# Kernel optimization log

Measured on AMD Instinct MI355X. Metric: run time of the kernel, lower is better.

Reference implementation:

```python
import jax, jax.numpy as jnp
import numpy as np

B, N, D = 4, 4096, 1024


def setup_inputs() -> dict:
    key = jax.random.key(0)
    ks = jax.random.split(key, 7)
    s = 1.0 / np.sqrt(D)
    return {
        "x": jax.random.normal(ks[0], (B, N, D), dtype=jnp.float32),
        "Wq": jax.random.uniform(ks[1], (D, D), jnp.float32, -s, s),
        "bq": jax.random.uniform(ks[2], (D,), jnp.float32, -s, s),
        "Wk": jax.random.uniform(ks[3], (D, D), jnp.float32, -s, s),
        "bk": jax.random.uniform(ks[4], (D,), jnp.float32, -s, s),
        "Wv": jax.random.uniform(ks[5], (D, D), jnp.float32, -s, s),
        "bv": jax.random.uniform(ks[6], (D,), jnp.float32, -s, s),
    }


def reference(x, Wq, bq, Wk, bk, Wv, bv):
    # Projections (nn.Linear: x @ W.T + b; here W stored as [in, out])
    Q = x @ Wq + bq
    K = x @ Wk + bk
    V = x @ Wv + bv
    Qp = jax.nn.elu(Q) + 1.0  # positive feature map
    Kp = jax.nn.elu(K) + 1.0
    KV = jnp.einsum('bnd,bne->bde', Kp, V)          # [B, D, D]
    numerator = jnp.einsum('bnd,bde->bne', Qp, KV)  # [B, N, D]
    K_sum = Kp.sum(axis=1)                           # [B, D]
    norm = jnp.einsum('bnd,bd->bn', Qp, K_sum)[..., None]
    eps = 1e-6
    return numerator / (norm + eps)
```

## Files before the change

### kernel.cpp

```cpp
#include <hip/hip_runtime.h>
#include <hip/hip_bf16.h>
#include <cstdint>

typedef __bf16 bf16x8 __attribute__((ext_vector_type(8)));
typedef float  f32x4  __attribute__((ext_vector_type(4)));
typedef unsigned short u16x8 __attribute__((ext_vector_type(8)));

__device__ __forceinline__ unsigned short f2bf(float f) {
  __hip_bfloat16 h = __float2bfloat16(f);
  return __builtin_bit_cast(unsigned short, h);
}
__device__ __forceinline__ float bf2f(unsigned short u) {
  return __builtin_bit_cast(float, (unsigned)u << 16);
}

#define GL2LDS16(gp, lp)                                                      \
  __builtin_amdgcn_global_load_lds(                                           \
      (const __attribute__((address_space(1))) unsigned int*)(gp),            \
      (__attribute__((address_space(3))) unsigned int*)(lp), 16, 0, 0)

#define SBAR                                                                  \
  {                                                                           \
    __builtin_amdgcn_s_barrier();                                             \
    __builtin_amdgcn_sched_barrier(0);                                        \
  }
#define WAITV(n)                                                              \
  {                                                                           \
    asm volatile("s_waitcnt vmcnt(" #n ")" ::: "memory");                     \
    __builtin_amdgcn_sched_barrier(0);                                        \
  }
#define WAITL0                                                                \
  {                                                                           \
    asm volatile("s_waitcnt lgkmcnt(0)" ::: "memory");                        \
    __builtin_amdgcn_sched_barrier(0);                                        \
  }

template <int MODE>
__global__ __launch_bounds__(1024, 4) void gemm256w(
    const unsigned short* __restrict__ A, long long lda, long long aOffZ,
    const unsigned short* __restrict__ B, long long ldb, long long bOffZ,
    void* __restrict__ C, long long ldc, long long cOffZ,
    const float* __restrict__ bias, const float* __restrict__ bias2,
    int K) {
  __shared__ __attribute__((aligned(16))) char lds[3 * 32768];
  const int t = threadIdx.x;
  const int wave = t >> 6, lane = t & 63;
  const int wm = wave >> 2, wn = wave & 3;
  const int fr = lane & 15, fq = lane >> 4;

  const int gx = gridDim.x, gy = gridDim.y;
  int flat = blockIdx.y * gx + blockIdx.x;
  const int total = gx * gy;
  if ((total & 7) == 0) flat = (flat & 7) * (total >> 3) + (flat >> 3);
  int bx, by;
  if (MODE == 1) {
    bx = flat / gy;
    by = flat - bx * gy;
  } else {
    bx = flat % gx;
    by = flat / gx;
  }
  const int m0 = by * 256, n0 = bx * 256;

  const long long z = blockIdx.z;
  long long aBase, bBase;
  if (MODE == 3) {
    const long long koff = (z & 3) * 4096 + (z >> 2) * 1024;
    aBase = koff;
    bBase = koff;
  } else {
    aBase = z * aOffZ;
    bBase = z * bOffZ;
  }
  const unsigned short* Az = A + aBase;
  const unsigned short* Bz = B + bBase;

  const unsigned short* gA;
  const unsigned short* gB;
  {
    int d = t * 16;
    int l = d ^ (((d >> 7) & 3) << 4);
    int row = l >> 6, kel = (l & 63) >> 1;
    gA = Az + (long long)(m0 + row) * lda + kel;
    gB = Bz + (long long)(n0 + row) * ldb + kel;
  }

  const int slotx = (fr >> 1) & 3;
  const int acore = wm * 4096 + fr * 64 + ((fq ^ slotx) << 4);
  const int bcore = 16384 + wn * 4096 + fr * 64 + ((fq ^ slotx) << 4);

  f32x4 acc[4][4];
#pragma unroll
  for (int i = 0; i < 4; ++i)
#pragma unroll
    for (int j = 0; j < 4; ++j) acc[i][j] = (f32x4){0.f, 0.f, 0.f, 0.f};

  const int NT = K >> 5;

  auto stage = [&](int tile) {
    char* sb = lds + (tile % 3) * 32768 + wave * 1024;
    const int k0 = tile << 5;
    GL2LDS16(gA + k0, sb);
    GL2LDS16(gB + k0, sb + 16384);
  };

  stage(0);
  stage(1);
  WAITV(2);
  SBAR;

  bf16x8 av[4], bv[4];
  for (int tt = 0; tt < NT - 2; ++tt) {
    const char* sb = lds + (tt % 3) * 32768;
    stage(tt + 2);
#pragma unroll
    for (int i = 0; i < 4; ++i) {
      av[i] = *(const bf16x8*)(sb + acore + i * 1024);
      bv[i] = *(const bf16x8*)(sb + bcore + i * 1024);
    }
    WAITL0;
    __builtin_amdgcn_s_setprio(1);
#pragma unroll
    for (int mi = 0; mi < 4; ++mi)
#pragma unroll
      for (int ni = 0; ni < 4; ++ni)
        acc[mi][ni] = __builtin_amdgcn_mfma_f32_16x16x32_bf16(
            av[mi], bv[ni], acc[mi][ni], 0, 0, 0);
    __builtin_amdgcn_s_setprio(0);
    WAITV(2);
    SBAR;
  }
  {
    const char* sb = lds + ((NT - 2) % 3) * 32768;
#pragma unroll
    for (int i = 0; i < 4; ++i) {
      av[i] = *(const bf16x8*)(sb + acore + i * 1024);
      bv[i] = *(const bf16x8*)(sb + bcore + i * 1024);
    }
    WAITL0;
#pragma unroll
    for (int mi = 0; mi < 4; ++mi)
#pragma unroll
      for (int ni = 0; ni < 4; ++ni)
        acc[mi][ni] = __builtin_amdgcn_mfma_f32_16x16x32_bf16(
            av[mi], bv[ni], acc[mi][ni], 0, 0, 0);
    WAITV(0);
    SBAR;
  }
  {
    const char* sb = lds + ((NT - 1) % 3) * 32768;
#pragma unroll
    for (int i = 0; i < 4; ++i) {
      av[i] = *(const bf16x8*)(sb + acore + i * 1024);
      bv[i] = *(const bf16x8*)(sb + bcore + i * 1024);
    }
    WAITL0;
#pragma unroll
    for (int mi = 0; mi < 4; ++mi)
#pragma unroll
      for (int ni = 0; ni < 4; ++ni)
        acc[mi][ni] = __builtin_amdgcn_mfma_f32_16x16x32_bf16(
            av[mi], bv[ni], acc[mi][ni], 0, 0, 0);
  }

  unsigned short* Cu = (unsigned short*)C + z * cOffZ;
  const bool lower = (m0 < 1024);
#pragma unroll
  for (int mi = 0; mi < 4; ++mi) {
    const int rbase = m0 + wm * 64 + mi * 16 + fq * 4;
    float rb[4];
#pragma unroll
    for (int j = 0; j < 4; ++j)
      if (MODE == 1) rb[j] = lower ? bias[rbase + j] : bias2[rbase - 1024 + j];
#pragma unroll
    for (int ni = 0; ni < 4; ++ni) {
      const int c = n0 + wn * 64 + ni * 16 + fr;
      float cb = 0.f;
      if (MODE == 0) cb = bias[c];
#pragma unroll
      for (int j = 0; j < 4; ++j) {
        float v = acc[mi][ni][j];
        if (MODE == 0) v += cb;
        if (MODE == 1) v += rb[j];
        if (MODE == 0 || (MODE == 1 && lower))
          v = (v > 0.f) ? v + 1.f : __expf(v);
        Cu[(long long)(rbase + j) * ldc + c] = f2bf(v);
      }
    }
  }
}

__global__ __launch_bounds__(512, 2) void gemm_num(
    const unsigned short* __restrict__ A, long long aOffZ,
    const unsigned short* __restrict__ B, long long bOffZ,
    float* __restrict__ C, long long cOffZ,
    const float* __restrict__ norm, long long normOffZ) {
  const long long lda = 1024, ldb = 1024, ldc = 1024;
  const int K = 1024;
  __shared__ __attribute__((aligned(16))) char lds[2 * 65536];
  const int t = threadIdx.x;
  const int wave = t >> 6, lane = t & 63;
  const int wm = wave >> 2, wn = wave & 3;
  const int fr = lane & 15, fq = lane >> 4;

  const int gx = gridDim.x, gy = gridDim.y;
  int flat = blockIdx.y * gx + blockIdx.x;
  const int total = gx * gy;
  if ((total & 7) == 0) flat = (flat & 7) * (total >> 3) + (flat >> 3);
  const int bx = flat % gx, by = flat / gx;
  const int m0 = by * 256, n0 = bx * 256;

  const long long z = blockIdx.z;
  const unsigned short* Az = A + z * aOffZ;
  const unsigned short* Bz = B + z * bOffZ;

  const unsigned short* gA[2];
  const unsigned short* gB[2];
#pragma unroll
  for (int c = 0; c < 2; ++c) {
    int d = c * 8192 + t * 16;
    int l = d ^ (((d >> 7) & 3) << 4);
    int row = l >> 6, kel = (l & 63) >> 1;
    gA[c] = Az + (long long)(m0 + row) * lda + kel;
    gB[c] = Bz + (long long)(n0 + row) * ldb + kel;
  }

  const int slotx = (fr >> 1) & 3;
  const int acore = wm * 8192 + fr * 64 + ((fq ^ slotx) << 4);
  const int bcore = wn * 4096 + fr * 64 + ((fq ^ slotx) << 4);

  f32x4 acc[8][4];
#pragma unroll
  for (int i = 0; i < 8; ++i)
#pragma unroll
    for (int j = 0; j < 4; ++j) acc[i][j] = (f32x4){0.f, 0.f, 0.f, 0.f};

  const int NT = K >> 6;

  auto stage_sub = [&](int tile, int which) {
    char* dst = lds + (tile & 1) * 65536 + which * 16384 + wave * 1024;
    const int kofs = (tile << 6) + ((which >> 1) << 5);
    if (which & 1) {
      GL2LDS16(gB[0] + kofs, dst);
      GL2LDS16(gB[1] + kofs, dst + 8192);
    } else {
      GL2LDS16(gA[0] + kofs, dst);
      GL2LDS16(gA[1] + kofs, dst + 8192);
    }
  };

  stage_sub(0, 0);
  stage_sub(0, 1);
  stage_sub(0, 2);
  stage_sub(0, 3);
  WAITV(4);
  SBAR;

  bf16x8 av[4], bv0[4], bv1[4];
  for (int tt = 0; tt < NT - 1; ++tt) {
    const char* bufp = lds + (tt & 1) * 65536;
#pragma unroll
    for (int i = 0; i < 4; ++i) {
      av[i] = *(const bf16x8*)(bufp + acore + i * 1024);
      bv0[i] = *(const bf16x8*)(bufp + 16384 + bcore + i * 1024);
    }
    stage_sub(tt + 1, 0);
    SBAR;
    WAITL0;
    __builtin_amdgcn_s_setprio(1);
#pragma unroll
    for (int mi = 0; mi < 4; ++mi)
#pragma unroll
      for (int ni = 0; ni < 4; ++ni)
        acc[mi][ni] = __builtin_amdgcn_mfma_f32_16x16x32_bf16(
            av[mi], bv0[ni], acc[mi][ni], 0, 0, 0);
    __builtin_amdgcn_s_setprio(0);
    SBAR;
#pragma unroll
    for (int i = 0; i < 4; ++i)
      av[i] = *(const bf16x8*)(bufp + acore + (4 + i) * 1024);
    stage_sub(tt + 1, 1);
    SBAR;
    WAITL0;
    __builtin_amdgcn_s_setprio(1);
#pragma unroll
    for (int mi = 0; mi < 4; ++mi)
#pragma unroll
      for (int ni = 0; ni < 4; ++ni)
        acc[4 + mi][ni] = __builtin_amdgcn_mfma_f32_16x16x32_bf16(
            av[mi], bv0[ni], acc[4 + mi][ni], 0, 0, 0);
    __builtin_amdgcn_s_setprio(0);
    WAITV(4);
    SBAR;
#pragma unroll
    for (int i = 0; i < 4; ++i) {
      av[i] = *(const bf16x8*)(bufp + 32768 + acore + i * 1024);
      bv1[i] = *(const bf16x8*)(bufp + 49152 + bcore + i * 1024);
    }
    stage_sub(tt + 1, 2);
    SBAR;
    WAITL0;
    __builtin_amdgcn_s_setprio(1);
#pragma unroll
    for (int mi = 0; mi < 4; ++mi)
#pragma unroll
      for (int ni = 0; ni < 4; ++ni)
        acc[mi][ni] = __builtin_amdgcn_mfma_f32_16x16x32_bf16(
            av[mi], bv1[ni], acc[mi][ni], 0, 0, 0);
    __builtin_amdgcn_s_setprio(0);
    SBAR;
#pragma unroll
    for (int i = 0; i < 4; ++i)
      av[i] = *(const bf16x8*)(bufp + 32768 + acore + (4 + i) * 1024);
    stage_sub(tt + 1, 3);
    SBAR;
    WAITL0;
    __builtin_amdgcn_s_setprio(1);
#pragma unroll
    for (int mi = 0; mi < 4; ++mi)
#pragma unroll
      for (int ni = 0; ni < 4; ++ni)
        acc[4 + mi][ni] = __builtin_amdgcn_mfma_f32_16x16x32_bf16(
            av[mi], bv1[ni], acc[4 + mi][ni], 0, 0, 0);
    __builtin_amdgcn_s_setprio(0);
    WAITV(4);
    SBAR;
  }
  {
    const char* bufp = lds + ((NT - 1) & 1) * 65536;
#pragma unroll
    for (int i = 0; i < 4; ++i) {
      av[i] = *(const bf16x8*)(bufp + acore + i * 1024);
      bv0[i] = *(const bf16x8*)(bufp + 16384 + bcore + i * 1024);
    }
    SBAR;
    WAITL0;
#pragma unroll
    for (int mi = 0; mi < 4; ++mi)
#pragma unroll
      for (int ni = 0; ni < 4; ++ni)
        acc[mi][ni] = __builtin_amdgcn_mfma_f32_16x16x32_bf16(
            av[mi], bv0[ni], acc[mi][ni], 0, 0, 0);
    SBAR;
#pragma unroll
    for (int i = 0; i < 4; ++i)
      av[i] = *(const bf16x8*)(bufp + acore + (4 + i) * 1024);
    SBAR;
    WAITL0;
#pragma unroll
    for (int mi = 0; mi < 4; ++mi)
#pragma unroll
      for (int ni = 0; ni < 4; ++ni)
        acc[4 + mi][ni] = __builtin_amdgcn_mfma_f32_16x16x32_bf16(
            av[mi], bv0[ni], acc[4 + mi][ni], 0, 0, 0);
    WAITV(0);
    SBAR;
#pragma unroll
    for (int i = 0; i < 4; ++i) {
      av[i] = *(const bf16x8*)(bufp + 32768 + acore + i * 1024);
      bv1[i] = *(const bf16x8*)(bufp + 49152 + bcore + i * 1024);
    }
    WAITL0;
#pragma unroll
    for (int mi = 0; mi < 4; ++mi)
#pragma unroll
      for (int ni = 0; ni < 4; ++ni)
        acc[mi][ni] = __builtin_amdgcn_mfma_f32_16x16x32_bf16(
            av[mi], bv1[ni], acc[mi][ni], 0, 0, 0);
#pragma unroll
    for (int i = 0; i < 4; ++i)
      av[i] = *(const bf16x8*)(bufp + 32768 + acore + (4 + i) * 1024);
    WAITL0;
#pragma unroll
    for (int mi = 0; mi < 4; ++mi)
#pragma unroll
      for (int ni = 0; ni < 4; ++ni)
        acc[4 + mi][ni] = __builtin_amdgcn_mfma_f32_16x16x32_bf16(
            av[mi], bv1[ni], acc[4 + mi][ni], 0, 0, 0);
  }

  const float* nrmz = norm + z * normOffZ;
  float* Cf = C + z * cOffZ;
#pragma unroll
  for (int mi = 0; mi < 8; ++mi) {
    const int rbase = m0 + wm * 128 + mi * 16 + fq * 4;
    float nv[4];
#pragma unroll
    for (int j = 0; j < 4; ++j) nv[j] = nrmz[rbase + j];
#pragma unroll
    for (int ni = 0; ni < 4; ++ni) {
      const int c = n0 + wn * 64 + ni * 16 + fr;
#pragma unroll
      for (int j = 0; j < 4; ++j)
        Cf[(long long)(rbase + j) * ldc + c] = acc[mi][ni][j] / nv[j];
    }
  }
}

__global__ __launch_bounds__(256) void reduce_kvt(
    const unsigned short* __restrict__ P, unsigned short* __restrict__ KVt) {
  const long long i = ((long long)blockIdx.x * 256 + threadIdx.x) * 8;
  const int b = (int)(i >> 20);
  const long long ed = i & ((1ll << 20) - 1);
  float s[8] = {0.f, 0.f, 0.f, 0.f, 0.f, 0.f, 0.f, 0.f};
#pragma unroll
  for (int ks = 0; ks < 4; ++ks) {
    u16x8 v = *(const u16x8*)(P + ((long long)(ks * 4 + b) << 20) + ed);
#pragma unroll
    for (int j = 0; j < 8; ++j) s[j] += bf2f(v[j]);
  }
  u16x8 o;
#pragma unroll
  for (int j = 0; j < 8; ++j) o[j] = f2bf(s[j]);
  *(u16x8*)(KVt + i) = o;
}

__global__ __launch_bounds__(256) void transpose_w(
    const float* __restrict__ W, unsigned short* __restrict__ WT) {
  __shared__ float tile[32][33];
  const int tx = threadIdx.x & 31, ty = threadIdx.x >> 5;
  const int i0 = blockIdx.y * 32, o0 = blockIdx.x * 32;
#pragma unroll
  for (int s = 0; s < 32; s += 8)
    tile[ty + s][tx] = W[(long long)(i0 + ty + s) * 1024 + o0 + tx];
  __syncthreads();
#pragma unroll
  for (int s = 0; s < 32; s += 8)
    WT[(long long)(o0 + ty + s) * 1024 + i0 + tx] = f2bf(tile[tx][ty + s]);
}

__global__ __launch_bounds__(256) void convert_x(
    const float4* __restrict__ in, uint2* __restrict__ out, int n4) {
  const int stride = gridDim.x * blockDim.x;
  for (int i = blockIdx.x * blockDim.x + threadIdx.x; i < n4; i += stride) {
    float4 v = in[i];
    uint2 o;
    o.x = (unsigned)f2bf(v.x) | ((unsigned)f2bf(v.y) << 16);
    o.y = (unsigned)f2bf(v.z) | ((unsigned)f2bf(v.w) << 16);
    out[i] = o;
  }
}

__global__ __launch_bounds__(256) void ksum_kernel(
    const unsigned short* __restrict__ KpT, float* __restrict__ Ksum) {
  const int gw = (blockIdx.x * 256 + threadIdx.x) >> 6;
  const int lane = threadIdx.x & 63;
  const int d = gw >> 2, b = gw & 3;
  const unsigned short* p = KpT + (long long)d * 16384 + b * 4096 + lane * 8;
  float s = 0.f;
#pragma unroll
  for (int it = 0; it < 8; ++it) {
    u16x8 v = *(const u16x8*)(p + it * 512);
#pragma unroll
    for (int j = 0; j < 8; ++j) s += bf2f(v[j]);
  }
#pragma unroll
  for (int o = 32; o > 0; o >>= 1) s += __shfl_down(s, o, 64);
  if (lane == 0) Ksum[b * 1024 + d] = s;
}

__global__ __launch_bounds__(256) void norm_kernel(
    const unsigned short* __restrict__ Qp, const float* __restrict__ Ksum,
    float* __restrict__ nrm) {
  const int gw = (blockIdx.x * 256 + threadIdx.x) >> 6;
  const int lane = threadIdx.x & 63;
  const int b = gw >> 12;
  const unsigned short* q = Qp + (long long)gw * 1024 + lane * 8;
  const float* ks = Ksum + b * 1024 + lane * 8;
  float s = 0.f;
#pragma unroll
  for (int it = 0; it < 2; ++it) {
    u16x8 v = *(const u16x8*)(q + it * 512);
    float4 k0 = *(const float4*)(ks + it * 512);
    float4 k1 = *(const float4*)(ks + it * 512 + 4);
    s += bf2f(v[0]) * k0.x + bf2f(v[1]) * k0.y + bf2f(v[2]) * k0.z +
         bf2f(v[3]) * k0.w + bf2f(v[4]) * k1.x + bf2f(v[5]) * k1.y +
         bf2f(v[6]) * k1.z + bf2f(v[7]) * k1.w;
  }
#pragma unroll
  for (int o = 32; o > 0; o >>= 1) s += __shfl_down(s, o, 64);
  if (lane == 0) nrm[gw] = s + 1e-6f;
}

extern "C" void kernel_launch(void* const* d_in, const int* in_sizes, int n_in,
                              void* d_out, int out_size, void* d_ws,
                              size_t ws_size, hipStream_t stream) {
  const float* x  = (const float*)d_in[0];
  const float* Wq = (const float*)d_in[1];
  const float* bq = (const float*)d_in[2];
  const float* Wk = (const float*)d_in[3];
  const float* bk = (const float*)d_in[4];
  const float* Wv = (const float*)d_in[5];
  const float* bv = (const float*)d_in[6];
  float* out = (float*)d_out;

  const size_t MN = 16384ull * 1024ull;
  char* w = (char*)d_ws;
  unsigned short* xb  = (unsigned short*)w;  w += MN * 2;
  unsigned short* WT  = (unsigned short*)w;  w += 3ull * 1024 * 1024 * 2;
  unsigned short* Qp  = (unsigned short*)w;  w += MN * 2;
  unsigned short* KVb = (unsigned short*)w;  w += 2 * MN * 2;
  unsigned short* KVt = (unsigned short*)w;  w += 4ull * 1024 * 1024 * 2;
  float* Ksum = (float*)w;  w += 4ull * 1024 * 4;
  float* nrm  = (float*)w;  w += 16384ull * 4;
  unsigned short* Pkv = xb;
  unsigned short* KpT = KVb;
  unsigned short* VT  = KVb + MN;

  transpose_w<<<dim3(32, 32), 256, 0, stream>>>(Wq, WT);
  transpose_w<<<dim3(32, 32), 256, 0, stream>>>(Wk, WT + 1024 * 1024);
  transpose_w<<<dim3(32, 32), 256, 0, stream>>>(Wv, WT + 2 * 1024 * 1024);
  convert_x<<<2048, 256, 0, stream>>>((const float4*)x, (uint2*)xb,
                                      (int)(MN / 4));

  gemm256w<0><<<dim3(4, 64, 1), 1024, 0, stream>>>(
      xb, 1024, 0, WT, 1024, 0, Qp, 1024, 0, bq, nullptr, 1024);
  gemm256w<1><<<dim3(64, 8, 1), 1024, 0, stream>>>(
      WT + 1024 * 1024, 1024, 0, xb, 1024, 0, KVb, 16384, 0, bk, bv, 1024);
  ksum_kernel<<<1024, 256, 0, stream>>>(KpT, Ksum);
  gemm256w<3><<<dim3(4, 4, 16), 1024, 0, stream>>>(
      VT, 16384, 0, KpT, 16384, 0, Pkv, 1024, 1024 * 1024, nullptr, nullptr,
      1024);
  reduce_kvt<<<2048, 256, 0, stream>>>(Pkv, KVt);
  norm_kernel<<<4096, 256, 0, stream>>>(Qp, Ksum, nrm);
  gemm_num<<<dim3(4, 16, 4), 512, 0, stream>>>(
      Qp, 4096ll * 1024, KVt, 1024 * 1024, out, 4096ll * 1024, nrm, 4096);
}
```

Baseline: 244.4 us.

## Merge independent kernels into combined launches to cut launch count

The three weight transposes and the x conversion now run as one grid. The Q and K/V projection GEMMs run as one 768-block launch, and the split-K reduction and norm computation share one tail kernel. GEMM templates are specialized into dedicated kernels with constant strides. The aim is to remove launch gaps and tail underutilization between small dependent-free kernels, at the cost of branchy blocks and possible resource or occupancy mismatch between the fused halves.

```diff
diff --git a/kernel.cpp b/kernel.cpp
--- a/kernel.cpp
+++ b/kernel.cpp
@@ -35,45 +35,44 @@
     __builtin_amdgcn_sched_barrier(0);                                        \
   }
 
-template <int MODE>
-__global__ __launch_bounds__(1024, 4) void gemm256w(
-    const unsigned short* __restrict__ A, long long lda, long long aOffZ,
-    const unsigned short* __restrict__ B, long long ldb, long long bOffZ,
-    void* __restrict__ C, long long ldc, long long cOffZ,
-    const float* __restrict__ bias, const float* __restrict__ bias2,
-    int K) {
+__global__ __launch_bounds__(1024, 4) void proj_fused(
+    const unsigned short* __restrict__ xb, const unsigned short* __restrict__ WT,
+    unsigned short* __restrict__ QpO, unsigned short* __restrict__ KVbO,
+    const float* __restrict__ bq, const float* __restrict__ bk,
+    const float* __restrict__ bv) {
   __shared__ __attribute__((aligned(16))) char lds[3 * 32768];
   const int t = threadIdx.x;
   const int wave = t >> 6, lane = t & 63;
   const int wm = wave >> 2, wn = wave & 3;
   const int fr = lane & 15, fq = lane >> 4;
 
-  const int gx = gridDim.x, gy = gridDim.y;
-  int flat = blockIdx.y * gx + blockIdx.x;
-  const int total = gx * gy;
-  if ((total & 7) == 0) flat = (flat & 7) * (total >> 3) + (flat >> 3);
-  int bx, by;
-  if (MODE == 1) {
-    bx = flat / gy;
-    by = flat - bx * gy;
+  const int h = blockIdx.x;
+  const bool kv = (h < 512);
+  const unsigned short* A;
+  const unsigned short* B;
+  unsigned short* Cc;
+  long long ldc;
+  int m0, n0;
+  if (kv) {
+    const int f = (h & 7) * 64 + (h >> 3);
+    const int bx = f >> 3, by = f & 7;
+    m0 = by * 256;
+    n0 = bx * 256;
+    A = WT + 1024 * 1024;
+    B = xb;
+    Cc = KVbO;
+    ldc = 16384;
   } else {
-    bx = flat % gx;
-    by = flat / gx;
-  }
-  const int m0 = by * 256, n0 = bx * 256;
-
-  const long long z = blockIdx.z;
-  long long aBase, bBase;
-  if (MODE == 3) {
-    const long long koff = (z & 3) * 4096 + (z >> 2) * 1024;
-    aBase = koff;
-    bBase = koff;
-  } else {
-    aBase = z * aOffZ;
-    bBase = z * bOffZ;
-  }
-  const unsigned short* Az = A + aBase;
-  const unsigned short* Bz = B + bBase;
+    const int hh = h - 512;
+    const int f = (hh & 7) * 32 + (hh >> 3);
+    const int bx = f & 3, by = f >> 2;
+    m0 = by * 256;
+    n0 = bx * 256;
+    A = xb;
+    B = WT;
+    Cc = QpO;
+    ldc = 1024;
+  }
 
   const unsigned short* gA;
   const unsigned short* gB;
@@ -81,8 +80,8 @@
     int d = t * 16;
     int l = d ^ (((d >> 7) & 3) << 4);
     int row = l >> 6, kel = (l & 63) >> 1;
-    gA = Az + (long long)(m0 + row) * lda + kel;
-    gB = Bz + (long long)(n0 + row) * ldb + kel;
+    gA = A + (long long)(m0 + row) * 1024 + kel;
+    gB = B + (long long)(n0 + row) * 1024 + kel;
   }
 
   const int slotx = (fr >> 1) & 3;
@@ -95,7 +94,7 @@
 #pragma unroll
     for (int j = 0; j < 4; ++j) acc[i][j] = (f32x4){0.f, 0.f, 0.f, 0.f};
 
-  const int NT = K >> 5;
+  const int NT = 32;
 
   auto stage = [&](int tile) {
     char* sb = lds + (tile % 3) * 32768 + wave * 1024;
@@ -109,6 +108,138 @@
   WAITV(2);
   SBAR;
 
+  bf16x8 av[4], bv4[4];
+  for (int tt = 0; tt < NT - 2; ++tt) {
+    const char* sb = lds + (tt % 3) * 32768;
+    stage(tt + 2);
+#pragma unroll
+    for (int i = 0; i < 4; ++i) {
+      av[i] = *(const bf16x8*)(sb + acore + i * 1024);
+      bv4[i] = *(const bf16x8*)(sb + bcore + i * 1024);
+    }
+    WAITL0;
+    __builtin_amdgcn_s_setprio(1);
+#pragma unroll
+    for (int mi = 0; mi < 4; ++mi)
+#pragma unroll
+      for (int ni = 0; ni < 4; ++ni)
+        acc[mi][ni] = __builtin_amdgcn_mfma_f32_16x16x32_bf16(
+            av[mi], bv4[ni], acc[mi][ni], 0, 0, 0);
+    __builtin_amdgcn_s_setprio(0);
+    WAITV(2);
+    SBAR;
+  }
+  {
+    const char* sb = lds + ((NT - 2) % 3) * 32768;
+#pragma unroll
+    for (int i = 0; i < 4; ++i) {
+      av[i] = *(const bf16x8*)(sb + acore + i * 1024);
+      bv4[i] = *(const bf16x8*)(sb + bcore + i * 1024);
+    }
+    WAITL0;
+#pragma unroll
+    for (int mi = 0; mi < 4; ++mi)
+#pragma unroll
+      for (int ni = 0; ni < 4; ++ni)
+        acc[mi][ni] = __builtin_amdgcn_mfma_f32_16x16x32_bf16(
+            av[mi], bv4[ni], acc[mi][ni], 0, 0, 0);
+    WAITV(0);
+    SBAR;
+  }
+  {
+    const char* sb = lds + ((NT - 1) % 3) * 32768;
+#pragma unroll
+    for (int i = 0; i < 4; ++i) {
+      av[i] = *(const bf16x8*)(sb + acore + i * 1024);
+      bv4[i] = *(const bf16x8*)(sb + bcore + i * 1024);
+    }
+    WAITL0;
+#pragma unroll
+    for (int mi = 0; mi < 4; ++mi)
+#pragma unroll
+      for (int ni = 0; ni < 4; ++ni)
+        acc[mi][ni] = __builtin_amdgcn_mfma_f32_16x16x32_bf16(
+            av[mi], bv4[ni], acc[mi][ni], 0, 0, 0);
+  }
+
+  const bool lower = (m0 < 1024);
+#pragma unroll
+  for (int mi = 0; mi < 4; ++mi) {
+    const int rbase = m0 + wm * 64 + mi * 16 + fq * 4;
+    float rb[4];
+#pragma unroll
+    for (int j = 0; j < 4; ++j)
+      if (kv) rb[j] = lower ? bk[rbase + j] : bv[rbase - 1024 + j];
+#pragma unroll
+    for (int ni = 0; ni < 4; ++ni) {
+      const int c = n0 + wn * 64 + ni * 16 + fr;
+      const float cb = kv ? 0.f : bq[c];
+#pragma unroll
+      for (int j = 0; j < 4; ++j) {
+        float v = acc[mi][ni][j];
+        v += kv ? rb[j] : cb;
+        if (!kv || lower) v = (v > 0.f) ? v + 1.f : __expf(v);
+        Cc[(long long)(rbase + j) * ldc + c] = f2bf(v);
+      }
+    }
+  }
+}
+
+__global__ __launch_bounds__(1024, 4) void gemm_splitk(
+    const unsigned short* __restrict__ A, const unsigned short* __restrict__ B,
+    unsigned short* __restrict__ C) {
+  __shared__ __attribute__((aligned(16))) char lds[3 * 32768];
+  const int t = threadIdx.x;
+  const int wave = t >> 6, lane = t & 63;
+  const int wm = wave >> 2, wn = wave & 3;
+  const int fr = lane & 15, fq = lane >> 4;
+
+  const int gx = gridDim.x, gy = gridDim.y;
+  int flat = blockIdx.y * gx + blockIdx.x;
+  const int total = gx * gy;
+  if ((total & 7) == 0) flat = (flat & 7) * (total >> 3) + (flat >> 3);
+  const int bx = flat % gx, by = flat / gx;
+  const int m0 = by * 256, n0 = bx * 256;
+
+  const long long z = blockIdx.z;
+  const long long koff = (z & 3) * 4096 + (z >> 2) * 1024;
+  const unsigned short* Az = A + koff;
+  const unsigned short* Bz = B + koff;
+
+  const unsigned short* gA;
+  const unsigned short* gB;
+  {
+    int d = t * 16;
+    int l = d ^ (((d >> 7) & 3) << 4);
+    int row = l >> 6, kel = (l & 63) >> 1;
+    gA = Az + (long long)(m0 + row) * 16384 + kel;
+    gB = Bz + (long long)(n0 + row) * 16384 + kel;
+  }
+
+  const int slotx = (fr >> 1) & 3;
+  const int acore = wm * 4096 + fr * 64 + ((fq ^ slotx) << 4);
+  const int bcore = 16384 + wn * 4096 + fr * 64 + ((fq ^ slotx) << 4);
+
+  f32x4 acc[4][4];
+#pragma unroll
+  for (int i = 0; i < 4; ++i)
+#pragma unroll
+    for (int j = 0; j < 4; ++j) acc[i][j] = (f32x4){0.f, 0.f, 0.f, 0.f};
+
+  const int NT = 32;
+
+  auto stage = [&](int tile) {
+    char* sb = lds + (tile % 3) * 32768 + wave * 1024;
+    const int k0 = tile << 5;
+    GL2LDS16(gA + k0, sb);
+    GL2LDS16(gB + k0, sb + 16384);
+  };
+
+  stage(0);
+  stage(1);
+  WAITV(2);
+  SBAR;
+
   bf16x8 av[4], bv[4];
   for (int tt = 0; tt < NT - 2; ++tt) {
     const char* sb = lds + (tt % 3) * 32768;
@@ -163,29 +294,16 @@
             av[mi], bv[ni], acc[mi][ni], 0, 0, 0);
   }
 
-  unsigned short* Cu = (unsigned short*)C + z * cOffZ;
-  const bool lower = (m0 < 1024);
+  unsigned short* Cu = C + z * 1048576ll;
 #pragma unroll
   for (int mi = 0; mi < 4; ++mi) {
     const int rbase = m0 + wm * 64 + mi * 16 + fq * 4;
-    float rb[4];
-#pragma unroll
-    for (int j = 0; j < 4; ++j)
-      if (MODE == 1) rb[j] = lower ? bias[rbase + j] : bias2[rbase - 1024 + j];
 #pragma unroll
     for (int ni = 0; ni < 4; ++ni) {
       const int c = n0 + wn * 64 + ni * 16 + fr;
-      float cb = 0.f;
-      if (MODE == 0) cb = bias[c];
-#pragma unroll
-      for (int j = 0; j < 4; ++j) {
-        float v = acc[mi][ni][j];
-        if (MODE == 0) v += cb;
-        if (MODE == 1) v += rb[j];
-        if (MODE == 0 || (MODE == 1 && lower))
-          v = (v > 0.f) ? v + 1.f : __expf(v);
-        Cu[(long long)(rbase + j) * ldc + c] = f2bf(v);
-      }
+#pragma unroll
+      for (int j = 0; j < 4; ++j)
+        Cu[(long long)(rbase + j) * 1024 + c] = f2bf(acc[mi][ni][j]);
     }
   }
 }
@@ -397,47 +515,33 @@
   }
 }
 
-__global__ __launch_bounds__(256) void reduce_kvt(
-    const unsigned short* __restrict__ P, unsigned short* __restrict__ KVt) {
-  const long long i = ((long long)blockIdx.x * 256 + threadIdx.x) * 8;
-  const int b = (int)(i >> 20);
-  const long long ed = i & ((1ll << 20) - 1);
-  float s[8] = {0.f, 0.f, 0.f, 0.f, 0.f, 0.f, 0.f, 0.f};
-#pragma unroll
-  for (int ks = 0; ks < 4; ++ks) {
-    u16x8 v = *(const u16x8*)(P + ((long long)(ks * 4 + b) << 20) + ed);
-#pragma unroll
-    for (int j = 0; j < 8; ++j) s[j] += bf2f(v[j]);
-  }
-  u16x8 o;
-#pragma unroll
-  for (int j = 0; j < 8; ++j) o[j] = f2bf(s[j]);
-  *(u16x8*)(KVt + i) = o;
-}
-
-__global__ __launch_bounds__(256) void transpose_w(
-    const float* __restrict__ W, unsigned short* __restrict__ WT) {
+__global__ __launch_bounds__(256) void prep_fused(
+    const float* __restrict__ Wq, const float* __restrict__ Wk,
+    const float* __restrict__ Wv, unsigned short* __restrict__ WT,
+    const float4* __restrict__ x4, uint2* __restrict__ xb4) {
   __shared__ float tile[32][33];
-  const int tx = threadIdx.x & 31, ty = threadIdx.x >> 5;
-  const int i0 = blockIdx.y * 32, o0 = blockIdx.x * 32;
-#pragma unroll
-  for (int s = 0; s < 32; s += 8)
-    tile[ty + s][tx] = W[(long long)(i0 + ty + s) * 1024 + o0 + tx];
-  __syncthreads();
-#pragma unroll
-  for (int s = 0; s < 32; s += 8)
-    WT[(long long)(o0 + ty + s) * 1024 + i0 + tx] = f2bf(tile[tx][ty + s]);
-}
-
-__global__ __launch_bounds__(256) void convert_x(
-    const float4* __restrict__ in, uint2* __restrict__ out, int n4) {
-  const int stride = gridDim.x * blockDim.x;
-  for (int i = blockIdx.x * blockDim.x + threadIdx.x; i < n4; i += stride) {
-    float4 v = in[i];
-    uint2 o;
-    o.x = (unsigned)f2bf(v.x) | ((unsigned)f2bf(v.y) << 16);
-    o.y = (unsigned)f2bf(v.z) | ((unsigned)f2bf(v.w) << 16);
-    out[i] = o;
+  if (blockIdx.z < 3) {
+    const float* W = blockIdx.z == 0 ? Wq : (blockIdx.z == 1 ? Wk : Wv);
+    unsigned short* out = WT + (size_t)blockIdx.z * 1024 * 1024;
+    const int tx = threadIdx.x & 31, ty = threadIdx.x >> 5;
+    const int i0 = blockIdx.y * 32, o0 = blockIdx.x * 32;
+#pragma unroll
+    for (int s = 0; s < 32; s += 8)
+      tile[ty + s][tx] = W[(long long)(i0 + ty + s) * 1024 + o0 + tx];
+    __syncthreads();
+#pragma unroll
+    for (int s = 0; s < 32; s += 8)
+      out[(long long)(o0 + ty + s) * 1024 + i0 + tx] = f2bf(tile[tx][ty + s]);
+  } else {
+    const int flat = blockIdx.y * 32 + blockIdx.x;
+    const int n4 = 4194304;
+    for (int i = flat * 256 + threadIdx.x; i < n4; i += 1024 * 256) {
+      float4 v = x4[i];
+      uint2 o;
+      o.x = (unsigned)f2bf(v.x) | ((unsigned)f2bf(v.y) << 16);
+      o.y = (unsigned)f2bf(v.z) | ((unsigned)f2bf(v.w) << 16);
+      xb4[i] = o;
+    }
   }
 }
 
@@ -459,27 +563,45 @@
   if (lane == 0) Ksum[b * 1024 + d] = s;
 }
 
-__global__ __launch_bounds__(256) void norm_kernel(
+__global__ __launch_bounds__(256) void tail_fused(
+    const unsigned short* __restrict__ P, unsigned short* __restrict__ KVt,
     const unsigned short* __restrict__ Qp, const float* __restrict__ Ksum,
     float* __restrict__ nrm) {
-  const int gw = (blockIdx.x * 256 + threadIdx.x) >> 6;
-  const int lane = threadIdx.x & 63;
-  const int b = gw >> 12;
-  const unsigned short* q = Qp + (long long)gw * 1024 + lane * 8;
-  const float* ks = Ksum + b * 1024 + lane * 8;
-  float s = 0.f;
-#pragma unroll
-  for (int it = 0; it < 2; ++it) {
-    u16x8 v = *(const u16x8*)(q + it * 512);
-    float4 k0 = *(const float4*)(ks + it * 512);
-    float4 k1 = *(const float4*)(ks + it * 512 + 4);
-    s += bf2f(v[0]) * k0.x + bf2f(v[1]) * k0.y + bf2f(v[2]) * k0.z +
-         bf2f(v[3]) * k0.w + bf2f(v[4]) * k1.x + bf2f(v[5]) * k1.y +
-         bf2f(v[6]) * k1.z + bf2f(v[7]) * k1.w;
-  }
-#pragma unroll
-  for (int o = 32; o > 0; o >>= 1) s += __shfl_down(s, o, 64);
-  if (lane == 0) nrm[gw] = s + 1e-6f;
+  if (blockIdx.x < 2048) {
+    const long long i = ((long long)blockIdx.x * 256 + threadIdx.x) * 8;
+    const int b = (int)(i >> 20);
+    const long long ed = i & ((1ll << 20) - 1);
+    float s[8] = {0.f, 0.f, 0.f, 0.f, 0.f, 0.f, 0.f, 0.f};
+#pragma unroll
+    for (int ks = 0; ks < 4; ++ks) {
+      u16x8 v = *(const u16x8*)(P + ((long long)(ks * 4 + b) << 20) + ed);
+#pragma unroll
+      for (int j = 0; j < 8; ++j) s[j] += bf2f(v[j]);
+    }
+    u16x8 o;
+#pragma unroll
+    for (int j = 0; j < 8; ++j) o[j] = f2bf(s[j]);
+    *(u16x8*)(KVt + i) = o;
+  } else {
+    const int gw = ((blockIdx.x - 2048) * 256 + threadIdx.x) >> 6;
+    const int lane = threadIdx.x & 63;
+    const int b = gw >> 12;
+    const unsigned short* q = Qp + (long long)gw * 1024 + lane * 8;
+    const float* ks = Ksum + b * 1024 + lane * 8;
+    float s = 0.f;
+#pragma unroll
+    for (int it = 0; it < 2; ++it) {
+      u16x8 v = *(const u16x8*)(q + it * 512);
+      float4 k0 = *(const float4*)(ks + it * 512);
+      float4 k1 = *(const float4*)(ks + it * 512 + 4);
+      s += bf2f(v[0]) * k0.x + bf2f(v[1]) * k0.y + bf2f(v[2]) * k0.z +
+           bf2f(v[3]) * k0.w + bf2f(v[4]) * k1.x + bf2f(v[5]) * k1.y +
+           bf2f(v[6]) * k1.z + bf2f(v[7]) * k1.w;
+    }
+#pragma unroll
+    for (int o = 32; o > 0; o >>= 1) s += __shfl_down(s, o, 64);
+    if (lane == 0) nrm[gw] = s + 1e-6f;
+  }
 }
 
 extern "C" void kernel_launch(void* const* d_in, const int* in_sizes, int n_in,
@@ -507,22 +629,12 @@
   unsigned short* KpT = KVb;
   unsigned short* VT  = KVb + MN;
 
-  transpose_w<<<dim3(32, 32), 256, 0, stream>>>(Wq, WT);
-  transpose_w<<<dim3(32, 32), 256, 0, stream>>>(Wk, WT + 1024 * 1024);
-  transpose_w<<<dim3(32, 32), 256, 0, stream>>>(Wv, WT + 2 * 1024 * 1024);
-  convert_x<<<2048, 256, 0, stream>>>((const float4*)x, (uint2*)xb,
-                                      (int)(MN / 4));
-
-  gemm256w<0><<<dim3(4, 64, 1), 1024, 0, stream>>>(
-      xb, 1024, 0, WT, 1024, 0, Qp, 1024, 0, bq, nullptr, 1024);
-  gemm256w<1><<<dim3(64, 8, 1), 1024, 0, stream>>>(
-      WT + 1024 * 1024, 1024, 0, xb, 1024, 0, KVb, 16384, 0, bk, bv, 1024);
+  prep_fused<<<dim3(32, 32, 4), 256, 0, stream>>>(Wq, Wk, Wv, WT,
+                                                  (const float4*)x, (uint2*)xb);
+  proj_fused<<<768, 1024, 0, stream>>>(xb, WT, Qp, KVb, bq, bk, bv);
   ksum_kernel<<<1024, 256, 0, stream>>>(KpT, Ksum);
-  gemm256w<3><<<dim3(4, 4, 16), 1024, 0, stream>>>(
-      VT, 16384, 0, KpT, 16384, 0, Pkv, 1024, 1024 * 1024, nullptr, nullptr,
-      1024);
-  reduce_kvt<<<2048, 256, 0, stream>>>(Pkv, KVt);
-  norm_kernel<<<4096, 256, 0, stream>>>(Qp, Ksum, nrm);
+  gemm_splitk<<<dim3(4, 4, 16), 1024, 0, stream>>>(VT, KpT, Pkv);
+  tail_fused<<<6144, 256, 0, stream>>>(Pkv, KVt, Qp, Ksum, nrm);
   gemm_num<<<dim3(4, 16, 4), 512, 0, stream>>>(
       Qp, 4096ll * 1024, KVt, 1024 * 1024, out, 4096ll * 1024, nrm, 4096);
 }
```

Measured after the change: 238.5 us. -2.4%, faster.
